# Optimization experiments

Measured on AMD Instinct MI355X. Metric: run time of the kernel, lower is better.

## Reference

```python
import jax, jax.numpy as jnp
import numpy as np

WINDOW_SIZE = 32  # band half-width = 16
EPS = 1e-5       # torch InstanceNorm1d default eps


def instance_norm_t(y):
    # y: (B, T, H); torch InstanceNorm1d (affine=False) normalizes each channel
    # over the temporal axis per sample, biased variance.
    m = jnp.mean(y, axis=1, keepdims=True)
    v = jnp.var(y, axis=1, keepdims=True)
    return (y - m) * jax.lax.rsqrt(v + EPS)


def setup_inputs() -> dict:
    key = jax.random.key(0)
    ks = jax.random.split(key, 7)
    B, T, IN, H = 4, 2048, 256, 256
    x = jax.random.normal(ks[0], (B, T, IN), dtype=jnp.float32)
    s = 0.02
    Wq = jax.random.normal(ks[1], (H, IN), dtype=jnp.float32) * s
    bq = jax.random.normal(ks[2], (H,), dtype=jnp.float32) * s
    Wk = jax.random.normal(ks[3], (H, IN), dtype=jnp.float32) * s
    bk = jax.random.normal(ks[4], (H,), dtype=jnp.float32) * s
    Wv = jax.random.normal(ks[5], (H, IN), dtype=jnp.float32) * s
    bv = jax.random.normal(ks[6], (H,), dtype=jnp.float32) * s
    return {"x": x, "Wq": Wq, "bq": bq, "Wk": Wk, "bk": bk, "Wv": Wv, "bv": bv}


def reference(x, Wq, bq, Wk, bk, Wv, bv):
    B, T, _ = x.shape
    H = Wq.shape[0]
    scale = H ** (-0.5)
    half = WINDOW_SIZE // 2  # 16

    q = instance_norm_t(x @ Wq.T + bq)  # (B, T, H)
    k = instance_norm_t(x @ Wk.T + bk)
    v = instance_norm_t(x @ Wv.T + bv)

    # Banded attention: for each query i only keys j with |i-j| <= half are live.
    offs = jnp.arange(-half, half + 1)                 # (W,) with W = 33
    idx = jnp.arange(T)[:, None] + offs[None, :]       # (T, W)
    valid = (idx >= 0) & (idx < T)                     # (T, W)
    idx_c = jnp.clip(idx, 0, T - 1)

    k_win = k[:, idx_c, :]                             # (B, T, W, H)
    v_win = v[:, idx_c, :]                             # (B, T, W, H)

    scores = jnp.einsum('bth,btwh->btw', q, k_win) * scale
    scores = jnp.where(valid[None], scores, -jnp.inf)
    probs = jax.nn.softmax(scores, axis=-1)            # (B, T, W)
    out = jnp.einsum('btw,btwh->bth', probs, v_win)    # (B, T, H)
    return jnp.mean(out, axis=1)                       # (B, H)
```

## Files before the change

### kernel.cpp

```cpp
#include <hip/hip_runtime.h>
#include <math.h>

#define BB 4
#define TT 2048
#define DIM 256
#define MROWS (BB*TT)
#define MN ((size_t)MROWS*DIM)
#define SCALE 0.0625f
#define HALF 16

typedef __attribute__((ext_vector_type(8))) short short8;
typedef __attribute__((ext_vector_type(4))) float f32x4;
typedef __attribute__((ext_vector_type(8))) unsigned short ushort8v;

__device__ __forceinline__ ushort f2bf(float f) {
    unsigned u = __builtin_bit_cast(unsigned, f);
    u += 0x7fffu + ((u >> 16) & 1u);
    return (ushort)(u >> 16);
}
__device__ __forceinline__ float bf2f(ushort u) {
    return __builtin_bit_cast(float, (unsigned)u << 16);
}
__device__ __forceinline__ unsigned cvtpk(float lo, float hi) {
    unsigned r;
    asm("v_cvt_pk_bf16_f32 %0, %1, %2" : "=v"(r) : "v"(lo), "v"(hi));
    return r;
}
__device__ __forceinline__ ushort8v pack8(f32x4 lo, f32x4 hi) {
    union { unsigned u[4]; ushort8v v; } r;
    r.u[0] = cvtpk(lo[0], lo[1]);
    r.u[1] = cvtpk(lo[2], lo[3]);
    r.u[2] = cvtpk(hi[0], hi[1]);
    r.u[3] = cvtpk(hi[2], hi[3]);
    return r.v;
}

#define GLOAD16(g, l) __builtin_amdgcn_global_load_lds( \
    (const __attribute__((address_space(1))) void*)(g), \
    (__attribute__((address_space(3))) void*)(l), 16, 0, 0)


#define A_TILE (128*64)
#define B_TILE (256*64)
__global__ __launch_bounds__(512) void gemm_kernel(
    const float* __restrict__ x,
    const float* __restrict__ Wq, const float* __restrict__ Wk, const float* __restrict__ Wv,
    const float* __restrict__ bq, const float* __restrict__ bk, const float* __restrict__ bv,
    ushort* __restrict__ qkv, float* __restrict__ part, float* __restrict__ out)
{
    __shared__ ushort As[2 * A_TILE];
    __shared__ ushort Bs[2 * B_TILE];
    __shared__ float sred[2][2][256];

    int tid = threadIdx.x;
    int lane = tid & 63, w = tid >> 6;
    int wr = w >> 2, wc = w & 3;

    int orig = blockIdx.x + blockIdx.y * 64;
    if (orig == 0) {
        out[tid] = 0.f; out[512 + tid] = 0.f;
    }

    int wg = (orig & 7) * 24 + (orig >> 3);
    int mb = wg / 3, nb = wg % 3;
    int m0 = mb * 128;
    int which = nb;

    const float* Wm   = which == 0 ? Wq : (which == 1 ? Wk : Wv);
    const float* bias = which == 0 ? bq : (which == 1 ? bk : bv);

    int srow = lane >> 3;
    int sc   = lane & 7;
    int kof  = (sc ^ srow) << 3;
    const float* aRow = x  + (size_t)(m0 + w * 16 + srow) * DIM + kof;
    const float* bRow = Wm + (size_t)(w * 32 + srow) * DIM + kof;
    int aBase = (w * 16 + srow) * 64 + sc * 8;
    int bBase = (w * 32 + srow) * 64 + sc * 8;

    f32x4 acc[4][4] = {};
    f32x4 ra[2][2], rb[4][2];

    auto loadT = [&](int kt) {
        int ko = kt * 64;
        #pragma unroll
        for (int g = 0; g < 2; g++) {
            ra[g][0] = *(const f32x4*)(aRow + (size_t)g * 8 * DIM + ko);
            ra[g][1] = *(const f32x4*)(aRow + (size_t)g * 8 * DIM + ko + 4);
        }
        #pragma unroll
        for (int g = 0; g < 4; g++) {
            rb[g][0] = *(const f32x4*)(bRow + (size_t)g * 8 * DIM + ko);
            rb[g][1] = *(const f32x4*)(bRow + (size_t)g * 8 * DIM + ko + 4);
        }
    };
    auto commitT = [&](int buf) {
        ushort* Ab = &As[buf * A_TILE];
        ushort* Bb = &Bs[buf * B_TILE];
        #pragma unroll
        for (int g = 0; g < 2; g++)
            *(ushort8v*)(&Ab[aBase + g * 8 * 64]) = pack8(ra[g][0], ra[g][1]);
        #pragma unroll
        for (int g = 0; g < 4; g++)
            *(ushort8v*)(&Bb[bBase + g * 8 * 64]) = pack8(rb[g][0], rb[g][1]);
    };

    int fr = lane & 15, fp = lane >> 4, swz = lane & 7;

    loadT(0);
    commitT(0);
    __syncthreads();
    int cur = 0;
    #pragma unroll
    for (int kt = 0; kt < 4; kt++) {
        if (kt < 3) loadT(kt + 1);
        const ushort* a_lds = &As[cur * A_TILE];
        const ushort* b_lds = &Bs[cur * B_TILE];
        #pragma unroll
        for (int ks = 0; ks < 2; ks++) {
            short8 af[4], bf[4];
            #pragma unroll
            for (int i = 0; i < 4; i++) {
                int row = wr * 64 + i * 16 + fr;
                int slot = ks * 4 + fp;
                af[i] = *(const short8*)(&a_lds[row * 64 + ((slot ^ swz) << 3)]);
            }
            #pragma unroll
            for (int j = 0; j < 4; j++) {
                int row = wc * 64 + j * 16 + fr;
                int slot = ks * 4 + fp;
                bf[j] = *(const short8*)(&b_lds[row * 64 + ((slot ^ swz) << 3)]);
            }
            #pragma unroll
            for (int i = 0; i < 4; i++)
                #pragma unroll
                for (int j = 0; j < 4; j++)
                    acc[i][j] = __builtin_amdgcn_mfma_f32_16x16x32_bf16(
                        af[i], bf[j], acc[i][j], 0, 0, 0);
        }
        if (kt < 3) commitT(cur ^ 1);
        __syncthreads();
        cur ^= 1;
    }

    int b_idx = mb >> 4;
    int mb_local = mb & 15;
    #pragma unroll
    for (int j = 0; j < 4; j++) {
        int col = wc * 64 + j * 16 + fr;
        float bb = bias[col];
        float s1 = 0.f, s2 = 0.f;
        ushort* outbase = qkv + (size_t)which * MN + col;
        #pragma unroll
        for (int i = 0; i < 4; i++) {
            #pragma unroll
            for (int rr = 0; rr < 4; rr++) {
                int row = m0 + wr * 64 + i * 16 + fp * 4 + rr;
                float y = acc[i][j][rr] + bb;
                ushort ub = f2bf(y);
                outbase[(size_t)row * DIM] = ub;
                float yr = bf2f(ub);
                s1 += yr; s2 += yr * yr;
            }
        }
        s1 += __shfl_xor(s1, 16, 64); s1 += __shfl_xor(s1, 32, 64);
        s2 += __shfl_xor(s2, 16, 64); s2 += __shfl_xor(s2, 32, 64);
        if (fp == 0) { sred[0][wr][col] = s1; sred[1][wr][col] = s2; }
    }
    __syncthreads();
    if (tid < 256) {
        float p1 = sred[0][0][tid] + sred[0][1][tid];
        float p2 = sred[1][0][tid] + sred[1][1][tid];
        int wb = which * 4 + b_idx;
        part[((size_t)(wb * 2 + 0) * 256 + tid) * 16 + mb_local] = p1;
        part[((size_t)(wb * 2 + 1) * 256 + tid) * 16 + mb_local] = p2;
    }
}

__global__ __launch_bounds__(256) void attn_kernel(const ushort* __restrict__ qkv,
                                                   const float* __restrict__ part,
                                                   float* __restrict__ out)
{
    int orig = blockIdx.x + blockIdx.y * 64;
    int wg = (orig & 7) * 32 + (orig >> 3);
    int tile = wg & 63, b = wg >> 6;
    int t0 = tile * 32;

    const ushort* qg = qkv;
    const ushort* kg = qkv + MN;
    const ushort* vg = qkv + 2 * MN;

    __shared__ ushort Qs[32 * 256];
    __shared__ ushort Ks[64 * 256];
    __shared__ float Ps[32][65];
    __shared__ float csp[4][64];
    __shared__ float qsc[256], qsh[256];

    int tid = threadIdx.x;
    int lane = tid & 63, w = tid >> 6;

    {
        int r0 = lane >> 5;
        int sp = lane & 31;
        #pragma unroll
        for (int i = 0; i < 8; i++) {
            int rowbase = (w * 8 + i) * 2;
            int r = rowbase + r0;
            int gt = t0 - HALF + r;
            int gtc = gt < 0 ? 0 : (gt > TT - 1 ? TT - 1 : gt);
            int s = sp ^ (r & 7);
            GLOAD16(kg + (size_t)(b * TT + gtc) * DIM + s * 8, &Ks[rowbase * 256]);
        }
    }

    float sums[3][2];
    #pragma unroll
    for (int wq = 0; wq < 3; wq++) {
        #pragma unroll
        for (int sm = 0; sm < 2; sm++) {
            const float* p = part + ((size_t)((wq * 4 + b) * 2 + sm) * 256 + tid) * 16;
            float a = 0.f;
            #pragma unroll
            for (int m4 = 0; m4 < 4; m4++) {
                f32x4 v = *(const f32x4*)(p + m4 * 4);
                a += (v[0] + v[1]) + (v[2] + v[3]);
            }
            sums[wq][sm] = a;
        }
    }
    float mq = sums[0][0] * (1.f / 2048.f);
    float rq = 1.f / sqrtf(sums[0][1] * (1.f / 2048.f) - mq * mq + 1e-5f);
    float mk = sums[1][0] * (1.f / 2048.f);
    float rk = 1.f / sqrtf(sums[1][1] * (1.f / 2048.f) - mk * mk + 1e-5f);
    float mv = sums[2][0] * (1.f / 2048.f);
    float rv = 1.f / sqrtf(sums[2][1] * (1.f / 2048.f) - mv * mv + 1e-5f);
    float qs = rq * rk;
    qsc[tid] = qs;  qsh[tid] = -mq * qs;
    float vscr = rv, vshr = -mv * rv;
    __syncthreads();

    #pragma unroll
    for (int i = 0; i < 4; i++) {
        int idx = tid + i * 256;
        int qr = idx >> 5, sp = idx & 31;
        int h0 = sp * 8;
        ushort8v raw = *(const ushort8v*)(qg + ((size_t)(b * TT + t0 + qr)) * DIM + h0);
        ushort8v o;
        #pragma unroll
        for (int e = 0; e < 8; e++)
            o[e] = f2bf(bf2f(raw[e]) * qsc[h0 + e] + qsh[h0 + e]);
        *(ushort8v*)(&Qs[qr * 256 + ((sp ^ (qr & 7)) << 3)]) = o;
    }
    __syncthreads();

    f32x4 sacc[2] = {};
    int fr = lane & 15, fp = lane >> 4, swz = lane & 7;
    int brow = w * 16 + fr;
    #pragma unroll
    for (int ks = 0; ks < 8; ks++) {
        int slot = ks * 4 + fp;
        short8 bfr = *(const short8*)(&Ks[brow * 256 + ((slot ^ swz) << 3)]);
        #pragma unroll
        for (int rf = 0; rf < 2; rf++) {
            int arow = rf * 16 + fr;
            short8 af = *(const short8*)(&Qs[arow * 256 + ((slot ^ swz) << 3)]);
            sacc[rf] = __builtin_amdgcn_mfma_f32_16x16x32_bf16(af, bfr, sacc[rf], 0, 0, 0);
        }
    }
    #pragma unroll
    for (int rf = 0; rf < 2; rf++)
        #pragma unroll
        for (int rr = 0; rr < 4; rr++)
            Ps[rf * 16 + fp * 4 + rr][w * 16 + fr] = sacc[rf][rr];
    __syncthreads();

    int r = tid >> 3, c0 = (tid & 7) * 8;
    float sv[8];
    float mx = -1e30f;
    #pragma unroll
    for (int j = 0; j < 8; j++) {
        int c = c0 + j;
        int gt = t0 - HALF + c;
        bool valid = (c >= r) && (c <= r + 32) && (gt >= 0) && (gt < TT);
        sv[j] = valid ? Ps[r][c] * SCALE : -1e30f;
        mx = fmaxf(mx, sv[j]);
    }
    #pragma unroll
    for (int d = 1; d < 8; d <<= 1) mx = fmaxf(mx, __shfl_xor(mx, d, 64));
    float sum = 0.f;
    #pragma unroll
    for (int j = 0; j < 8; j++) { sv[j] = __expf(sv[j] - mx); sum += sv[j]; }
    #pragma unroll
    for (int d = 1; d < 8; d <<= 1) sum += __shfl_xor(sum, d, 64);
    float inv = 1.0f / sum;
    #pragma unroll
    for (int j = 0; j < 8; j++) Ps[r][c0 + j] = sv[j] * inv;
    __syncthreads();

    {
        int c = tid & 63, rq4 = tid >> 6;
        float s = 0.f;
        #pragma unroll
        for (int j = 0; j < 8; j++) s += Ps[rq4 * 8 + j][c];
        csp[rq4][c] = s;
    }
    __syncthreads();

    int h = tid;
    const ushort* vrow = vg + (size_t)b * TT * DIM + h;
    float o = 0.f;
    #pragma unroll 8
    for (int c = 0; c < 64; c++) {
        float cs = csp[0][c] + csp[1][c] + csp[2][c] + csp[3][c];
        int gt = t0 - HALF + c;
        int gtc = gt < 0 ? 0 : (gt > TT - 1 ? TT - 1 : gt);
        o += cs * bf2f(vrow[(size_t)gtc * DIM]);
    }
    o = vscr * o + 32.f * vshr;
    atomicAdd(&out[(size_t)b * DIM + h], o * (1.0f / TT));
}

extern "C" void kernel_launch(void* const* d_in, const int* in_sizes, int n_in,
                              void* d_out, int out_size, void* d_ws, size_t ws_size,
                              hipStream_t stream) {
    const float* x  = (const float*)d_in[0];
    const float* Wq = (const float*)d_in[1];
    const float* bq = (const float*)d_in[2];
    const float* Wk = (const float*)d_in[3];
    const float* bk = (const float*)d_in[4];
    const float* Wv = (const float*)d_in[5];
    const float* bv = (const float*)d_in[6];
    float* out = (float*)d_out;

    ushort* qkv  = (ushort*)d_ws;
    float* part  = (float*)(qkv + 3 * MN);

    gemm_kernel<<<dim3(64, 3), 512, 0, stream>>>(x, Wq, Wk, Wv, bq, bk, bv, qkv, part, out);
    attn_kernel<<<dim3(64, 4), 256, 0, stream>>>(qkv, part, out);
}
```

Baseline: 25.03 us.

## Double GEMM block to 1024 threads and stage bf16 output through LDS for coalesced stores

The QKV GEMM block grows from 8 to 16 waves, so each wave now computes a 32x64 sub-tile instead of 64x64. This halves per-wave accumulators and raises latency hiding per CU. The epilogue writes bf16 results into a padded LDS tile and then copies them out with 16-byte coalesced global stores, replacing scattered 2-byte strided stores. The statistics reduction now sums four row-waves instead of two, and LDS is reused through a single aliased buffer. The tile-buffer aliasing relies on the loop's final barrier, and the copy-out needs a barrier that the existing sync provides.

```diff
diff --git a/kernel.cpp b/kernel.cpp
--- a/kernel.cpp
+++ b/kernel.cpp
@@ -40,26 +40,22 @@
     (__attribute__((address_space(3))) void*)(l), 16, 0, 0)
 
 
-#define A_TILE (128*64)
-#define B_TILE (256*64)
-__global__ __launch_bounds__(512) void gemm_kernel(
+#define AT (128*64)
+#define BT (256*64)
+__global__ __launch_bounds__(1024) void gemm_kernel(
     const float* __restrict__ x,
     const float* __restrict__ Wq, const float* __restrict__ Wk, const float* __restrict__ Wv,
     const float* __restrict__ bq, const float* __restrict__ bk, const float* __restrict__ bv,
     ushort* __restrict__ qkv, float* __restrict__ part, float* __restrict__ out)
 {
-    __shared__ ushort As[2 * A_TILE];
-    __shared__ ushort Bs[2 * B_TILE];
-    __shared__ float sred[2][2][256];
+    __shared__ ushort lds[2 * AT + 2 * BT];
 
     int tid = threadIdx.x;
     int lane = tid & 63, w = tid >> 6;
     int wr = w >> 2, wc = w & 3;
 
     int orig = blockIdx.x + blockIdx.y * 64;
-    if (orig == 0) {
-        out[tid] = 0.f; out[512 + tid] = 0.f;
-    }
+    if (orig == 0) out[tid] = 0.f;
 
     int wg = (orig & 7) * 24 + (orig >> 3);
     int mb = wg / 3, nb = wg % 3;
@@ -72,35 +68,30 @@
     int srow = lane >> 3;
     int sc   = lane & 7;
     int kof  = (sc ^ srow) << 3;
-    const float* aRow = x  + (size_t)(m0 + w * 16 + srow) * DIM + kof;
-    const float* bRow = Wm + (size_t)(w * 32 + srow) * DIM + kof;
-    int aBase = (w * 16 + srow) * 64 + sc * 8;
-    int bBase = (w * 32 + srow) * 64 + sc * 8;
-
-    f32x4 acc[4][4] = {};
-    f32x4 ra[2][2], rb[4][2];
+    const float* aRow = x  + (size_t)(m0 + w * 8 + srow) * DIM + kof;
+    const float* bRow = Wm + (size_t)(w * 16 + srow) * DIM + kof;
+    int aBase = (w * 8 + srow) * 64 + sc * 8;
+    int bBase = (w * 16 + srow) * 64 + sc * 8;
+
+    f32x4 acc[2][4] = {};
+    f32x4 ra[2], rb[2][2];
 
     auto loadT = [&](int kt) {
         int ko = kt * 64;
+        ra[0] = *(const f32x4*)(aRow + ko);
+        ra[1] = *(const f32x4*)(aRow + ko + 4);
         #pragma unroll
         for (int g = 0; g < 2; g++) {
-            ra[g][0] = *(const f32x4*)(aRow + (size_t)g * 8 * DIM + ko);
-            ra[g][1] = *(const f32x4*)(aRow + (size_t)g * 8 * DIM + ko + 4);
-        }
-        #pragma unroll
-        for (int g = 0; g < 4; g++) {
             rb[g][0] = *(const f32x4*)(bRow + (size_t)g * 8 * DIM + ko);
             rb[g][1] = *(const f32x4*)(bRow + (size_t)g * 8 * DIM + ko + 4);
         }
     };
     auto commitT = [&](int buf) {
-        ushort* Ab = &As[buf * A_TILE];
-        ushort* Bb = &Bs[buf * B_TILE];
+        ushort* Ab = &lds[buf * AT];
+        ushort* Bb = &lds[2 * AT + buf * BT];
+        *(ushort8v*)(&Ab[aBase]) = pack8(ra[0], ra[1]);
         #pragma unroll
         for (int g = 0; g < 2; g++)
-            *(ushort8v*)(&Ab[aBase + g * 8 * 64]) = pack8(ra[g][0], ra[g][1]);
-        #pragma unroll
-        for (int g = 0; g < 4; g++)
             *(ushort8v*)(&Bb[bBase + g * 8 * 64]) = pack8(rb[g][0], rb[g][1]);
     };
 
@@ -113,14 +104,14 @@
     #pragma unroll
     for (int kt = 0; kt < 4; kt++) {
         if (kt < 3) loadT(kt + 1);
-        const ushort* a_lds = &As[cur * A_TILE];
-        const ushort* b_lds = &Bs[cur * B_TILE];
+        const ushort* a_lds = &lds[cur * AT];
+        const ushort* b_lds = &lds[2 * AT + cur * BT];
         #pragma unroll
         for (int ks = 0; ks < 2; ks++) {
-            short8 af[4], bf[4];
-            #pragma unroll
-            for (int i = 0; i < 4; i++) {
-                int row = wr * 64 + i * 16 + fr;
+            short8 af[2], bf[4];
+            #pragma unroll
+            for (int i = 0; i < 2; i++) {
+                int row = wr * 32 + i * 16 + fr;
                 int slot = ks * 4 + fp;
                 af[i] = *(const short8*)(&a_lds[row * 64 + ((slot ^ swz) << 3)]);
             }
@@ -131,7 +122,7 @@
                 bf[j] = *(const short8*)(&b_lds[row * 64 + ((slot ^ swz) << 3)]);
             }
             #pragma unroll
-            for (int i = 0; i < 4; i++)
+            for (int i = 0; i < 2; i++)
                 #pragma unroll
                 for (int j = 0; j < 4; j++)
                     acc[i][j] = __builtin_amdgcn_mfma_f32_16x16x32_bf16(
@@ -142,6 +133,8 @@
         cur ^= 1;
     }
 
+    float* sred = (float*)lds;
+    ushort* T   = lds + 4096;
     int b_idx = mb >> 4;
     int mb_local = mb & 15;
     #pragma unroll
@@ -149,30 +142,42 @@
         int col = wc * 64 + j * 16 + fr;
         float bb = bias[col];
         float s1 = 0.f, s2 = 0.f;
-        ushort* outbase = qkv + (size_t)which * MN + col;
-        #pragma unroll
-        for (int i = 0; i < 4; i++) {
+        #pragma unroll
+        for (int i = 0; i < 2; i++) {
             #pragma unroll
             for (int rr = 0; rr < 4; rr++) {
-                int row = m0 + wr * 64 + i * 16 + fp * 4 + rr;
+                int rl = wr * 32 + i * 16 + fp * 4 + rr;
                 float y = acc[i][j][rr] + bb;
                 ushort ub = f2bf(y);
-                outbase[(size_t)row * DIM] = ub;
+                T[rl * 264 + col] = ub;
                 float yr = bf2f(ub);
                 s1 += yr; s2 += yr * yr;
             }
         }
         s1 += __shfl_xor(s1, 16, 64); s1 += __shfl_xor(s1, 32, 64);
         s2 += __shfl_xor(s2, 16, 64); s2 += __shfl_xor(s2, 32, 64);
-        if (fp == 0) { sred[0][wr][col] = s1; sred[1][wr][col] = s2; }
+        if (fp == 0) {
+            sred[(0 * 4 + wr) * 256 + col] = s1;
+            sred[(1 * 4 + wr) * 256 + col] = s2;
+        }
     }
     __syncthreads();
     if (tid < 256) {
-        float p1 = sred[0][0][tid] + sred[0][1][tid];
-        float p2 = sred[1][0][tid] + sred[1][1][tid];
+        float p1 = sred[0 * 1024 + 0 * 256 + tid] + sred[0 * 1024 + 1 * 256 + tid]
+                 + sred[0 * 1024 + 2 * 256 + tid] + sred[0 * 1024 + 3 * 256 + tid];
+        float p2 = sred[1 * 1024 + 0 * 256 + tid] + sred[1 * 1024 + 1 * 256 + tid]
+                 + sred[1 * 1024 + 2 * 256 + tid] + sred[1 * 1024 + 3 * 256 + tid];
         int wb = which * 4 + b_idx;
         part[((size_t)(wb * 2 + 0) * 256 + tid) * 16 + mb_local] = p1;
         part[((size_t)(wb * 2 + 1) * 256 + tid) * 16 + mb_local] = p2;
+    }
+    ushort* qbase = qkv + (size_t)which * MN + (size_t)m0 * DIM;
+    #pragma unroll
+    for (int g = 0; g < 4; g++) {
+        int task = tid + g * 1024;
+        int rl = task >> 5, sl = task & 31;
+        ushort8v v = *(const ushort8v*)(&T[rl * 264 + sl * 8]);
+        *(ushort8v*)(qbase + (size_t)rl * DIM + sl * 8) = v;
     }
 }
 
@@ -334,6 +339,6 @@
     ushort* qkv  = (ushort*)d_ws;
     float* part  = (float*)(qkv + 3 * MN);
 
-    gemm_kernel<<<dim3(64, 3), 512, 0, stream>>>(x, Wq, Wk, Wv, bq, bk, bv, qkv, part, out);
+    gemm_kernel<<<dim3(64, 3), 1024, 0, stream>>>(x, Wq, Wk, Wv, bq, bk, bv, qkv, part, out);
     attn_kernel<<<dim3(64, 4), 256, 0, stream>>>(qkv, part, out);
 }
```

Result: no change. 25.35 us (+1.3%).

## Retile fused QKV GEMM to 192-wide N tiles and prefetch V into LDS

Applied to the files above, without the earlier changes.

The GEMM now treats Q, K and V as one 768-column output and splits it into four 192-wide N tiles. This raises the grid from 192 to 256 workgroups so the CUs are filled more evenly, with weight and bias rows picked per row group across the three matrices. The attention kernel now asynchronously loads the V window into LDS next to K, and precomputes the column sums of the probabilities once. This replaces strided global V reads in the final reduction loop, at the cost of 32 KB more LDS per block.

```diff
diff --git a/kernel.cpp b/kernel.cpp
--- a/kernel.cpp
+++ b/kernel.cpp
@@ -41,7 +41,7 @@
 
 
 #define A_TILE (128*64)
-#define B_TILE (256*64)
+#define B_TILE (192*64)
 __global__ __launch_bounds__(512) void gemm_kernel(
     const float* __restrict__ x,
     const float* __restrict__ Wq, const float* __restrict__ Wk, const float* __restrict__ Wv,
@@ -50,35 +50,38 @@
 {
     __shared__ ushort As[2 * A_TILE];
     __shared__ ushort Bs[2 * B_TILE];
-    __shared__ float sred[2][2][256];
+    __shared__ float sred[2][2][192];
 
     int tid = threadIdx.x;
     int lane = tid & 63, w = tid >> 6;
     int wr = w >> 2, wc = w & 3;
 
-    int orig = blockIdx.x + blockIdx.y * 64;
+    int orig = blockIdx.x;
     if (orig == 0) {
         out[tid] = 0.f; out[512 + tid] = 0.f;
     }
 
-    int wg = (orig & 7) * 24 + (orig >> 3);
-    int mb = wg / 3, nb = wg % 3;
-    int m0 = mb * 128;
-    int which = nb;
-
-    const float* Wm   = which == 0 ? Wq : (which == 1 ? Wk : Wv);
-    const float* bias = which == 0 ? bq : (which == 1 ? bk : bv);
+    int wg = (orig & 7) * 32 + (orig >> 3);
+    int mb = wg >> 2, nt = wg & 3;
+    int m0 = mb * 128, n0 = nt * 192;
 
     int srow = lane >> 3;
     int sc   = lane & 7;
     int kof  = (sc ^ srow) << 3;
-    const float* aRow = x  + (size_t)(m0 + w * 16 + srow) * DIM + kof;
-    const float* bRow = Wm + (size_t)(w * 32 + srow) * DIM + kof;
+    const float* aRow = x + (size_t)(m0 + w * 16 + srow) * DIM + kof;
+    const float* bRowP[3];
+    #pragma unroll
+    for (int g = 0; g < 3; g++) {
+        int grow = n0 + w * 24 + g * 8 + srow;
+        int whr = grow >> 8;
+        const float* Wr = whr == 0 ? Wq : (whr == 1 ? Wk : Wv);
+        bRowP[g] = Wr + (size_t)(grow & 255) * DIM + kof;
+    }
     int aBase = (w * 16 + srow) * 64 + sc * 8;
-    int bBase = (w * 32 + srow) * 64 + sc * 8;
-
-    f32x4 acc[4][4] = {};
-    f32x4 ra[2][2], rb[4][2];
+    int bBase = (w * 24 + srow) * 64 + sc * 8;
+
+    f32x4 acc[4][3] = {};
+    f32x4 ra[2][2], rb[3][2];
 
     auto loadT = [&](int kt) {
         int ko = kt * 64;
@@ -88,9 +91,9 @@
             ra[g][1] = *(const f32x4*)(aRow + (size_t)g * 8 * DIM + ko + 4);
         }
         #pragma unroll
-        for (int g = 0; g < 4; g++) {
-            rb[g][0] = *(const f32x4*)(bRow + (size_t)g * 8 * DIM + ko);
-            rb[g][1] = *(const f32x4*)(bRow + (size_t)g * 8 * DIM + ko + 4);
+        for (int g = 0; g < 3; g++) {
+            rb[g][0] = *(const f32x4*)(bRowP[g] + ko);
+            rb[g][1] = *(const f32x4*)(bRowP[g] + ko + 4);
         }
     };
     auto commitT = [&](int buf) {
@@ -100,7 +103,7 @@
         for (int g = 0; g < 2; g++)
             *(ushort8v*)(&Ab[aBase + g * 8 * 64]) = pack8(ra[g][0], ra[g][1]);
         #pragma unroll
-        for (int g = 0; g < 4; g++)
+        for (int g = 0; g < 3; g++)
             *(ushort8v*)(&Bb[bBase + g * 8 * 64]) = pack8(rb[g][0], rb[g][1]);
     };
 
@@ -117,7 +120,7 @@
         const ushort* b_lds = &Bs[cur * B_TILE];
         #pragma unroll
         for (int ks = 0; ks < 2; ks++) {
-            short8 af[4], bf[4];
+            short8 af[4], bf[3];
             #pragma unroll
             for (int i = 0; i < 4; i++) {
                 int row = wr * 64 + i * 16 + fr;
@@ -125,15 +128,15 @@
                 af[i] = *(const short8*)(&a_lds[row * 64 + ((slot ^ swz) << 3)]);
             }
             #pragma unroll
-            for (int j = 0; j < 4; j++) {
-                int row = wc * 64 + j * 16 + fr;
+            for (int j = 0; j < 3; j++) {
+                int row = wc * 48 + j * 16 + fr;
                 int slot = ks * 4 + fp;
                 bf[j] = *(const short8*)(&b_lds[row * 64 + ((slot ^ swz) << 3)]);
             }
             #pragma unroll
             for (int i = 0; i < 4; i++)
                 #pragma unroll
-                for (int j = 0; j < 4; j++)
+                for (int j = 0; j < 3; j++)
                     acc[i][j] = __builtin_amdgcn_mfma_f32_16x16x32_bf16(
                         af[i], bf[j], acc[i][j], 0, 0, 0);
         }
@@ -145,11 +148,16 @@
     int b_idx = mb >> 4;
     int mb_local = mb & 15;
     #pragma unroll
-    for (int j = 0; j < 4; j++) {
-        int col = wc * 64 + j * 16 + fr;
-        float bb = bias[col];
+    for (int j = 0; j < 3; j++) {
+        int lstart = wc * 48 + j * 16;
+        int gstart = n0 + lstart;
+        int whf = gstart >> 8;
+        int hbase = gstart & 255;
+        const float* bias = whf == 0 ? bq : (whf == 1 ? bk : bv);
+        int h = hbase + fr;
+        float bb = bias[h];
         float s1 = 0.f, s2 = 0.f;
-        ushort* outbase = qkv + (size_t)which * MN + col;
+        ushort* outbase = qkv + (size_t)whf * MN + h;
         #pragma unroll
         for (int i = 0; i < 4; i++) {
             #pragma unroll
@@ -164,15 +172,17 @@
         }
         s1 += __shfl_xor(s1, 16, 64); s1 += __shfl_xor(s1, 32, 64);
         s2 += __shfl_xor(s2, 16, 64); s2 += __shfl_xor(s2, 32, 64);
-        if (fp == 0) { sred[0][wr][col] = s1; sred[1][wr][col] = s2; }
-    }
-    __syncthreads();
-    if (tid < 256) {
+        if (fp == 0) { sred[0][wr][lstart + fr] = s1; sred[1][wr][lstart + fr] = s2; }
+    }
+    __syncthreads();
+    if (tid < 192) {
         float p1 = sred[0][0][tid] + sred[0][1][tid];
         float p2 = sred[1][0][tid] + sred[1][1][tid];
-        int wb = which * 4 + b_idx;
-        part[((size_t)(wb * 2 + 0) * 256 + tid) * 16 + mb_local] = p1;
-        part[((size_t)(wb * 2 + 1) * 256 + tid) * 16 + mb_local] = p2;
+        int gcol = n0 + tid;
+        int whc = gcol >> 8, h = gcol & 255;
+        int wb = whc * 4 + b_idx;
+        part[((size_t)(wb * 2 + 0) * 256 + h) * 16 + mb_local] = p1;
+        part[((size_t)(wb * 2 + 1) * 256 + h) * 16 + mb_local] = p2;
     }
 }
 
@@ -191,8 +201,10 @@
 
     __shared__ ushort Qs[32 * 256];
     __shared__ ushort Ks[64 * 256];
+    __shared__ ushort Vs[64 * 256];
     __shared__ float Ps[32][65];
     __shared__ float csp[4][64];
+    __shared__ float csum[64];
     __shared__ float qsc[256], qsh[256];
 
     int tid = threadIdx.x;
@@ -209,6 +221,7 @@
             int gtc = gt < 0 ? 0 : (gt > TT - 1 ? TT - 1 : gt);
             int s = sp ^ (r & 7);
             GLOAD16(kg + (size_t)(b * TT + gtc) * DIM + s * 8, &Ks[rowbase * 256]);
+            GLOAD16(vg + (size_t)(b * TT + gtc) * DIM + sp * 8, &Vs[rowbase * 256]);
         }
     }
 
@@ -304,17 +317,14 @@
         csp[rq4][c] = s;
     }
     __syncthreads();
+    if (tid < 64) csum[tid] = csp[0][tid] + csp[1][tid] + csp[2][tid] + csp[3][tid];
+    __syncthreads();
 
     int h = tid;
-    const ushort* vrow = vg + (size_t)b * TT * DIM + h;
     float o = 0.f;
     #pragma unroll 8
-    for (int c = 0; c < 64; c++) {
-        float cs = csp[0][c] + csp[1][c] + csp[2][c] + csp[3][c];
-        int gt = t0 - HALF + c;
-        int gtc = gt < 0 ? 0 : (gt > TT - 1 ? TT - 1 : gt);
-        o += cs * bf2f(vrow[(size_t)gtc * DIM]);
-    }
+    for (int c = 0; c < 64; c++)
+        o += csum[c] * bf2f(Vs[c * 256 + h]);
     o = vscr * o + 32.f * vshr;
     atomicAdd(&out[(size_t)b * DIM + h], o * (1.0f / TT));
 }
@@ -334,6 +344,6 @@
     ushort* qkv  = (ushort*)d_ws;
     float* part  = (float*)(qkv + 3 * MN);
 
-    gemm_kernel<<<dim3(64, 3), 512, 0, stream>>>(x, Wq, Wk, Wv, bq, bk, bv, qkv, part, out);
+    gemm_kernel<<<dim3(256), 512, 0, stream>>>(x, Wq, Wk, Wv, bq, bk, bv, qkv, part, out);
     attn_kernel<<<dim3(64, 4), 256, 0, stream>>>(qkv, part, out);
 }
```

Result: faster. 23.75 us (-5.1%).
